# Optimization experiments

Measured on AMD Instinct MI355X. Metric: run time of the kernel, lower is better.

Reference implementation:

```python
import jax, jax.numpy as jnp
import numpy as np

D_EMBED = 64
N_HEADS = 4
D_HEAD = D_EMBED // N_HEADS
D_FF = 96          # int(1.5 * d_embed)
D_MODEL = 128      # repeat_factor = d_model // d_embed = 2
EPS = 1e-5
B = 4
# (idx_start, kernel_size, channels_in, kernel_no) per layer of the source CNN
LAYERS = [(0, 9, 8, 256), (18688, 9, 16, 256), (55808, 9, 16, 512)]
N_PARAMS = 130048
MAX_SEQ = max(ks * cin for _, ks, cin, _ in LAYERS) + 1  # 145


def _kernel_indices(start, ks, cin, kno):
    # Static ragged slice indices: per kernel, its weights plus trailing bias.
    L = ks * cin
    base = start + np.arange(kno)[:, None] * L + np.arange(L)[None, :]
    bias = start + kno * L + np.arange(kno)
    return np.concatenate([base, bias[:, None]], axis=1)  # (kno, L+1)


_IDX = [jnp.asarray(_kernel_indices(*l)) for l in LAYERS]


def setup_inputs():
    key = jax.random.key(0)
    k = jax.random.split(key, 8)
    s = 1.0 / np.sqrt(D_EMBED)
    return {
        "x": jax.random.normal(k[0], (B, N_PARAMS), dtype=jnp.float32),
        "pos_emb": jax.random.normal(k[1], (MAX_SEQ, D_EMBED), dtype=jnp.float32) * s,
        "comp_token": jax.random.normal(k[2], (D_EMBED,), dtype=jnp.float32),
        "in_proj_w": jax.random.normal(k[3], (3 * D_EMBED, D_EMBED), dtype=jnp.float32) * s,
        "in_proj_b": jnp.zeros((3 * D_EMBED,), jnp.float32),
        "out_proj_w": jax.random.normal(k[4], (D_EMBED, D_EMBED), dtype=jnp.float32) * s,
        "out_proj_b": jnp.zeros((D_EMBED,), jnp.float32),
        "lin1_w": jax.random.normal(k[5], (D_FF, D_EMBED), dtype=jnp.float32) * s,
        "lin1_b": jnp.zeros((D_FF,), jnp.float32),
        "lin2_w": jax.random.normal(k[6], (D_EMBED, D_FF), dtype=jnp.float32) / np.sqrt(D_FF),
        "lin2_b": jnp.zeros((D_EMBED,), jnp.float32),
        "ln1_w": jnp.ones((D_EMBED,), jnp.float32),
        "ln1_b": jnp.zeros((D_EMBED,), jnp.float32),
        "ln2_w": jnp.ones((D_EMBED,), jnp.float32),
        "ln2_b": jnp.zeros((D_EMBED,), jnp.float32),
    }


def _layernorm(x, w, b):
    mu = jnp.mean(x, axis=-1, keepdims=True)
    var = jnp.mean(jnp.square(x - mu), axis=-1, keepdims=True)
    return (x - mu) * jax.lax.rsqrt(var + EPS) * w + b


def _encoder(t, in_proj_w, in_proj_b, out_proj_w, out_proj_b,
             lin1_w, lin1_b, lin2_w, lin2_b, ln1_w, ln1_b, ln2_w, ln2_b):
    # Post-norm TransformerEncoderLayer (relu, eval mode -> dropout = identity).
    M, S, _ = t.shape
    qkv = t @ in_proj_w.T + in_proj_b                     # (M, S, 3D)
    q, k, v = jnp.split(qkv, 3, axis=-1)
    heads = lambda u: u.reshape(M, S, N_HEADS, D_HEAD).transpose(0, 2, 1, 3)
    q, k, v = heads(q), heads(k), heads(v)
    attn = jax.nn.softmax(jnp.einsum('mhsd,mhtd->mhst', q, k) / np.sqrt(D_HEAD))
    o = jnp.einsum('mhst,mhtd->mhsd', attn, v).transpose(0, 2, 1, 3).reshape(M, S, D_EMBED)
    o = o @ out_proj_w.T + out_proj_b
    h = _layernorm(t + o, ln1_w, ln1_b)
    ff = jax.nn.relu(h @ lin1_w.T + lin1_b) @ lin2_w.T + lin2_b
    return _layernorm(h + ff, ln2_w, ln2_b)


def reference(x, pos_emb, comp_token, in_proj_w, in_proj_b, out_proj_w, out_proj_b,
              lin1_w, lin1_b, lin2_w, lin2_b, ln1_w, ln1_b, ln2_w, ln2_b):
    enc = (in_proj_w, in_proj_b, out_proj_w, out_proj_b,
           lin1_w, lin1_b, lin2_w, lin2_b, ln1_w, ln1_b, ln2_w, ln2_b)
    outs = []
    for idx in _IDX:  # fixed small loop over layers; kernels within a layer are batched
        K, n = idx.shape
        w = x[:, idx]                                     # (B, K, n) ragged gather
        tok = w[..., None] + pos_emb[:n]                  # scalar -> d_embed broadcast + pos add
        cls = jnp.broadcast_to(comp_token, (B, K, 1, D_EMBED))
        tok = jnp.concatenate([cls, tok], axis=2).reshape(B * K, n + 1, D_EMBED)
        y = _encoder(tok, *enc)[:, 0, :]                  # comp-token readout
        outs.append(y.reshape(B, K, D_EMBED))
    y = jnp.concatenate(outs, axis=1)                     # (B, 1024, d_embed)
    return jnp.tile(y, (1, 1, D_MODEL // D_EMBED))        # (B, 1024, d_model)
```

## Files before the change

### kernel.cpp

```cpp
#include <hip/hip_runtime.h>
#include <math.h>

#define NPAR 130048
#define EPSF 1e-5f

#define VSTR  148
#define WSTR  68
#define L2STR 100

#define OFF_VPOST 0
#define OFF_WO    (64*VSTR)
#define OFF_L1    (OFF_WO + 64*WSTR)
#define OFF_L2    (OFF_L1 + 96*WSTR)
#define OFF_BETA  (OFF_L2 + 64*L2STR)
#define OFF_SM    (OFF_BETA + 4*VSTR)
#define SM_CT   0
#define SM_BO   64
#define SM_B1   128
#define SM_B2   224
#define SM_LN1W 288
#define SM_LN1B 352
#define SM_LN2W 416
#define SM_LN2B 480
#define SM_VCLS 544
#define SM_UV   608
#define SM_ALGA 672
#define SM_SIZE 680
#define SHARED_FLOATS (OFF_SM + SM_SIZE)

#define PW_W    0
#define PW_O    VSTR
#define PW_H1   (VSTR+64)
#define PW_R    (VSTR+128)
#define PW_ATT  (VSTR+224)
#define PW_SIZE (VSTR+224+2*VSTR)
#define LDS_FLOATS (SHARED_FLOATS + 16*PW_SIZE)

#define WSV 0
#define WSB (64*VSTR)
#define WSC (WSB + 4*VSTR)
#define WS_TOTAL (WSC + 136)

#define WAVE_SYNC() asm volatile("s_waitcnt lgkmcnt(0)" ::: "memory")

__device__ __forceinline__ unsigned short f2b(float f) {
    unsigned u = __float_as_uint(f);
    return (unsigned short)((u + 0x7fffu + ((u >> 16) & 1u)) >> 16);
}

__global__ __launch_bounds__(64) void k_pre(const float* __restrict__ pe,
                                            const float* __restrict__ ct,
                                            const float* __restrict__ W,
                                            const float* __restrict__ bq,
                                            float* __restrict__ ws)
{
    const int j = blockIdx.x;
    const int o = threadIdx.x;
    const float4* wq4 = (const float4*)(W + o*64);
    const float4* wk4 = (const float4*)(W + (64 + o)*64);
    const float4* wv4 = (const float4*)(W + (128 + o)*64);
    const float4* ct4 = (const float4*)ct;

    if (j < 145) {
        const float4* p4 = (const float4*)(pe + j*64);
        float sk = bq[64 + o], sv = bq[128 + o], sq = bq[o];
        #pragma unroll
        for (int e = 0; e < 16; ++e) {
            float4 k4 = wk4[e], v4 = wv4[e], q4 = wq4[e], pp = p4[e], cc = ct4[e];
            sk += k4.x*pp.x + k4.y*pp.y + k4.z*pp.z + k4.w*pp.w;
            sv += v4.x*pp.x + v4.y*pp.y + v4.z*pp.z + v4.w*pp.w;
            sq += q4.x*cc.x + q4.y*cc.y + q4.z*cc.z + q4.w*cc.w;
        }
        ws[WSV + o*VSTR + j] = sv;
        float r = sq * sk;
        #pragma unroll
        for (int off = 1; off < 16; off <<= 1) r += __shfl_xor(r, off);
        if ((o & 15) == 0) ws[WSB + (o >> 4)*VSTR + j] = r;
    } else {
        float sq = bq[o], sk = bq[64 + o], sv = bq[128 + o], suk = 0.f, suv = 0.f;
        #pragma unroll
        for (int e = 0; e < 16; ++e) {
            float4 k4 = wk4[e], v4 = wv4[e], q4 = wq4[e], cc = ct4[e];
            sq += q4.x*cc.x + q4.y*cc.y + q4.z*cc.z + q4.w*cc.w;
            sk += k4.x*cc.x + k4.y*cc.y + k4.z*cc.z + k4.w*cc.w;
            sv += v4.x*cc.x + v4.y*cc.y + v4.z*cc.z + v4.w*cc.w;
            suk += k4.x + k4.y + k4.z + k4.w;
            suv += v4.x + v4.y + v4.z + v4.w;
        }
        ws[WSC + o]      = sv;
        ws[WSC + 64 + o] = suv;
        ws[WSV + o*VSTR + 145] = 0.f;
        ws[WSV + o*VSTR + 146] = 0.f;
        ws[WSV + o*VSTR + 147] = 0.f;
        float a = sq * suk, g = sq * sk;
        #pragma unroll
        for (int off = 1; off < 16; off <<= 1) {
            a += __shfl_xor(a, off);
            g += __shfl_xor(g, off);
        }
        if ((o & 15) == 0) { ws[WSC + 128 + (o >> 4)] = a; ws[WSC + 128 + 4 + (o >> 4)] = g; }
    }
}

template<int L>
__device__ __forceinline__ void seq_compute(
    const float* __restrict__ xb, int start, int kno, int k, int lane,
    const float* __restrict__ lds, float* __restrict__ pw,
    float* __restrict__ po)
{
    constexpr int N  = L + 1;
    constexpr int S  = N + 1;
    constexpr int NS = (S + 15) / 16;
    constexpr int N4 = (N + 3) / 4;

    const float* sm = lds + OFF_SM;
    float* w_s = pw + PW_W;
    unsigned short* au = (unsigned short*)(pw + PW_ATT);

    if (lane * 4 < L) {
        float4 v = *(const float4*)(xb + start + (size_t)k * L + lane*4);
        *(float4*)(w_s + lane*4) = v;
    }
    if (lane == 0) w_s[L] = xb[start + (size_t)kno * L + k];
    WAVE_SYNC();

    const int e = lane & 15;
    const int h = lane >> 4;
    const float alpha = sm[SM_ALGA + h];
    const float gam   = sm[SM_ALGA + 4 + h];
    const float* bh   = lds + OFF_BETA + h*VSTR;

    float p[NS];
    float m = -1e30f;
    #pragma unroll
    for (int t = 0; t < NS; ++t) {
        const int s = e + 16*t;
        float v = -1e30f;
        if (s < S) {
            v = (s == 0) ? gam : fmaf(alpha, w_s[s-1], bh[s-1]);
            v *= 0.25f;
        }
        p[t] = v;
        m = fmaxf(m, v);
    }
    #pragma unroll
    for (int off = 1; off < 16; off <<= 1) m = fmaxf(m, __shfl_xor(m, off));

    float sum = 0.f;
    #pragma unroll
    for (int t = 0; t < NS; ++t) {
        const int s = e + 16*t;
        if (s < S) { float ex = __expf(p[t] - m); p[t] = ex; sum += ex; }
    }
    #pragma unroll
    for (int off = 1; off < 16; off <<= 1) sum += __shfl_xor(sum, off);
    const float inv = 1.f / sum;

    float wsl = 0.f;
    #pragma unroll
    for (int t = 0; t < NS; ++t) {
        const int s = e + 16*t;
        if (s > 0 && s < S) {
            float a = p[t] * inv;
            au[h*VSTR + (s-1)] = f2b(a);
            wsl += a * w_s[s-1];
        }
    }
    #pragma unroll
    for (int off = 1; off < 16; off <<= 1) wsl += __shfl_xor(wsl, off);
    const float wsum = wsl;
    const float a0 = __shfl(p[0] * inv, lane & 48);
    { int jj = N + e; if (jj < 4*N4) au[h*VSTR + jj] = 0; }
    WAVE_SYNC();

    const int d = lane;
    {
        const float4* vrow = (const float4*)(lds + OFF_VPOST + d*VSTR);
        const unsigned short* ah = au + h*VSTR;
        float c0 = 0.f, c1 = 0.f, c2 = 0.f, c3 = 0.f;
        #pragma unroll
        for (int t = 0; t < N4; ++t) {
            uint2 aa = *(const uint2*)(ah + 4*t);
            float4 v = vrow[t];
            c0 += __uint_as_float(aa.x << 16)          * v.x;
            c1 += __uint_as_float(aa.x & 0xffff0000u)  * v.y;
            c2 += __uint_as_float(aa.y << 16)          * v.z;
            c3 += __uint_as_float(aa.y & 0xffff0000u)  * v.w;
        }
        pw[PW_O + d] = (c0 + c1) + (c2 + c3) + wsum*sm[SM_UV + d] + a0*sm[SM_VCLS + d];
    }
    WAVE_SYNC();

    float op = sm[SM_BO + d];
    {
        const float4* wr = (const float4*)(lds + OFF_WO + d*WSTR);
        const float4* os = (const float4*)(pw + PW_O);
        float ax=0, ay=0, az=0, aw=0;
        #pragma unroll
        for (int t = 0; t < 16; ++t) {
            float4 w4 = wr[t], o4 = os[t];
            ax += w4.x*o4.x; ay += w4.y*o4.y; az += w4.z*o4.z; aw += w4.w*o4.w;
        }
        op += (ax + ay) + (az + aw);
    }
    float pre = sm[SM_CT + d] + op;
    float mu = pre;
    #pragma unroll
    for (int off = 32; off; off >>= 1) mu += __shfl_xor(mu, off);
    mu *= (1.f/64.f);
    float dv = pre - mu;
    float var = dv*dv;
    #pragma unroll
    for (int off = 32; off; off >>= 1) var += __shfl_xor(var, off);
    var *= (1.f/64.f);
    float h1 = dv * rsqrtf(var + EPSF) * sm[SM_LN1W + d] + sm[SM_LN1B + d];
    pw[PW_H1 + d] = h1;
    WAVE_SYNC();

    {
        const float4* hv = (const float4*)(pw + PW_H1);
        {
            const float4* r1 = (const float4*)(lds + OFF_L1 + lane*WSTR);
            float ax=0, ay=0, az=0, aw=0;
            #pragma unroll
            for (int t = 0; t < 16; ++t) {
                float4 w4 = r1[t], h4 = hv[t];
                ax += w4.x*h4.x; ay += w4.y*h4.y; az += w4.z*h4.z; aw += w4.w*h4.w;
            }
            pw[PW_R + lane] = fmaxf(sm[SM_B1 + lane] + (ax+ay) + (az+aw), 0.f);
        }
        if (lane < 32) {
            const float4* r1 = (const float4*)(lds + OFF_L1 + (64 + lane)*WSTR);
            float ax=0, ay=0, az=0, aw=0;
            #pragma unroll
            for (int t = 0; t < 16; ++t) {
                float4 w4 = r1[t], h4 = hv[t];
                ax += w4.x*h4.x; ay += w4.y*h4.y; az += w4.z*h4.z; aw += w4.w*h4.w;
            }
            pw[PW_R + 64 + lane] = fmaxf(sm[SM_B1 + 64 + lane] + (ax+ay) + (az+aw), 0.f);
        }
    }
    WAVE_SYNC();

    float f2 = sm[SM_B2 + d];
    {
        const float4* r2 = (const float4*)(lds + OFF_L2 + d*L2STR);
        const float4* rv = (const float4*)(pw + PW_R);
        float ax=0, ay=0, az=0, aw=0;
        #pragma unroll
        for (int t = 0; t < 24; ++t) {
            float4 w4 = r2[t], h4 = rv[t];
            ax += w4.x*h4.x; ay += w4.y*h4.y; az += w4.z*h4.z; aw += w4.w*h4.w;
        }
        f2 += (ax + ay) + (az + aw);
    }
    float pre2 = h1 + f2;
    float mu2 = pre2;
    #pragma unroll
    for (int off = 32; off; off >>= 1) mu2 += __shfl_xor(mu2, off);
    mu2 *= (1.f/64.f);
    float dv2 = pre2 - mu2;
    float var2 = dv2*dv2;
    #pragma unroll
    for (int off = 32; off; off >>= 1) var2 += __shfl_xor(var2, off);
    var2 *= (1.f/64.f);
    float y = dv2 * rsqrtf(var2 + EPSF) * sm[SM_LN2W + d] + sm[SM_LN2B + d];

    po[d]      = y;
    po[64 + d] = y;
}

__global__ __launch_bounds__(1024, 4) void k_main(
    const float* __restrict__ x,
    const float* __restrict__ ct,
    const float* __restrict__ Wo,  const float* __restrict__ bo,
    const float* __restrict__ L1w, const float* __restrict__ b1,
    const float* __restrict__ L2w, const float* __restrict__ b2,
    const float* __restrict__ ln1w, const float* __restrict__ ln1b,
    const float* __restrict__ ln2w, const float* __restrict__ ln2b,
    const float* __restrict__ ws,
    float* __restrict__ out)
{
    __shared__ float lds[LDS_FLOATS];
    const int tid = threadIdx.x;

    {
        const float4* s4 = (const float4*)(ws + WSV);
        float4* d4 = (float4*)(lds + OFF_VPOST);
        for (int i = tid; i < 2368; i += 1024) d4[i] = s4[i];
        if (tid < 148) ((float4*)(lds + OFF_BETA))[tid] = ((const float4*)(ws + WSB))[tid];
        for (int idx = tid; idx < 4096; idx += 1024)
            lds[OFF_WO + (idx >> 6)*WSTR + (idx & 63)] = Wo[idx];
        for (int idx = tid; idx < 6144; idx += 1024)
            lds[OFF_L1 + (idx >> 6)*WSTR + (idx & 63)] = L1w[idx];
        for (int idx = tid; idx < 6144; idx += 1024) {
            int r = idx / 96, c = idx - r*96;
            lds[OFF_L2 + r*L2STR + c] = L2w[idx];
        }
        if (tid < 64) {
            lds[OFF_SM + SM_CT   + tid] = ct[tid];
            lds[OFF_SM + SM_BO   + tid] = bo[tid];
            lds[OFF_SM + SM_B2   + tid] = b2[tid];
            lds[OFF_SM + SM_LN1W + tid] = ln1w[tid];
            lds[OFF_SM + SM_LN1B + tid] = ln1b[tid];
            lds[OFF_SM + SM_LN2W + tid] = ln2w[tid];
            lds[OFF_SM + SM_LN2B + tid] = ln2b[tid];
        } else if (tid < 256) {
            int t = tid - 64;
            if (t < 96) lds[OFF_SM + SM_B1 + t] = b1[t];
        } else if (tid < 392) {
            int t = tid - 256;
            lds[OFF_SM + SM_VCLS + t] = ws[WSC + t];
        }
    }
    __syncthreads();

    const int wave = tid >> 6;
    const int lane = tid & 63;
    float* pw = lds + SHARED_FLOATS + wave * PW_SIZE;
    int g = wave * 256 + blockIdx.x;

    if (wave < 4) {
        int b = g >> 8, k = g & 255;
        seq_compute<72>(x + (size_t)b*NPAR, 0, 256, k, lane, lds, pw,
                        out + ((size_t)b*1024 + k)*128);
    } else if (wave < 8) {
        g -= 1024; int b = g >> 8, k = g & 255;
        seq_compute<144>(x + (size_t)b*NPAR, 18688, 256, k, lane, lds, pw,
                         out + ((size_t)b*1024 + 256 + k)*128);
    } else {
        g -= 2048; int b = g >> 9, k = g & 511;
        seq_compute<144>(x + (size_t)b*NPAR, 55808, 512, k, lane, lds, pw,
                         out + ((size_t)b*1024 + 512 + k)*128);
    }
}

extern "C" void kernel_launch(void* const* d_in, const int* in_sizes, int n_in,
                              void* d_out, int out_size, void* d_ws, size_t ws_size,
                              hipStream_t stream) {
    const float* x    = (const float*)d_in[0];
    const float* pe   = (const float*)d_in[1];
    const float* ct   = (const float*)d_in[2];
    const float* Wq   = (const float*)d_in[3];
    const float* bq   = (const float*)d_in[4];
    const float* Wo   = (const float*)d_in[5];
    const float* bo   = (const float*)d_in[6];
    const float* L1w  = (const float*)d_in[7];
    const float* b1   = (const float*)d_in[8];
    const float* L2w  = (const float*)d_in[9];
    const float* b2   = (const float*)d_in[10];
    const float* ln1w = (const float*)d_in[11];
    const float* ln1b = (const float*)d_in[12];
    const float* ln2w = (const float*)d_in[13];
    const float* ln2b = (const float*)d_in[14];
    float* out = (float*)d_out;
    float* ws  = (float*)d_ws;

    k_pre <<<146, 64, 0, stream>>>(pe, ct, Wq, bq, ws);
    k_main<<<256, 1024, 0, stream>>>(x, ct, Wo, bo, L1w, b1, L2w, b2,
                                     ln1w, ln1b, ln2w, ln2b, ws, out);
}
```

Measured before the change: 23.15 us.

## Store weights and activations as fp16 in LDS and use packed dot2

```diff
diff --git a/kernel.cpp b/kernel.cpp
--- a/kernel.cpp
+++ b/kernel.cpp
@@ -4,16 +4,30 @@
 #define NPAR 130048
 #define EPSF 1e-5f
 
-#define VSTR  148
-#define WSTR  68
-#define L2STR 100
+typedef _Float16 hfp;
+typedef _Float16 h2 __attribute__((ext_vector_type(2)));
+
+#if defined(__has_builtin)
+#if __has_builtin(__builtin_amdgcn_fdot2)
+#define FDOT2(a,b,c) __builtin_amdgcn_fdot2((a),(b),(c),false)
+#endif
+#endif
+#ifndef FDOT2
+#define FDOT2(a,b,c) ((float)(a).x*(float)(b).x + (float)(a).y*(float)(b).y + (c))
+#endif
+
+__device__ __forceinline__ h2 f2h2(float f) { union { float f; h2 h; } u; u.f = f; return u.h; }
+
+#define VSTRH  152
+#define WSTRH  72
+#define L2STRH 104
 
 #define OFF_VPOST 0
-#define OFF_WO    (64*VSTR)
-#define OFF_L1    (OFF_WO + 64*WSTR)
-#define OFF_L2    (OFF_L1 + 96*WSTR)
-#define OFF_BETA  (OFF_L2 + 64*L2STR)
-#define OFF_SM    (OFF_BETA + 4*VSTR)
+#define OFF_WO    4864
+#define OFF_L1    7168
+#define OFF_L2    10624
+#define OFF_BETA  13952
+#define OFF_SM    14560
 #define SM_CT   0
 #define SM_BO   64
 #define SM_B1   128
@@ -25,28 +39,21 @@
 #define SM_VCLS 544
 #define SM_UV   608
 #define SM_ALGA 672
-#define SM_SIZE 680
-#define SHARED_FLOATS (OFF_SM + SM_SIZE)
+#define SHARED_FLOATS 15240
 
 #define PW_W    0
-#define PW_O    VSTR
-#define PW_H1   (VSTR+64)
-#define PW_R    (VSTR+128)
-#define PW_ATT  (VSTR+224)
-#define PW_SIZE (VSTR+224+2*VSTR)
+#define PW_O    152
+#define PW_H1   184
+#define PW_R    216
+#define PW_ATT  264
+#define PW_SIZE 568
 #define LDS_FLOATS (SHARED_FLOATS + 16*PW_SIZE)
 
-#define WSV 0
-#define WSB (64*VSTR)
-#define WSC (WSB + 4*VSTR)
-#define WS_TOTAL (WSC + 136)
+#define WSV_F 0
+#define WSB_F 4864
+#define WSC_F 5472
 
 #define WAVE_SYNC() asm volatile("s_waitcnt lgkmcnt(0)" ::: "memory")
-
-__device__ __forceinline__ unsigned short f2b(float f) {
-    unsigned u = __float_as_uint(f);
-    return (unsigned short)((u + 0x7fffu + ((u >> 16) & 1u)) >> 16);
-}
 
 __global__ __launch_bounds__(64) void k_pre(const float* __restrict__ pe,
                                             const float* __restrict__ ct,
@@ -60,6 +67,7 @@
     const float4* wk4 = (const float4*)(W + (64 + o)*64);
     const float4* wv4 = (const float4*)(W + (128 + o)*64);
     const float4* ct4 = (const float4*)ct;
+    hfp* wsh = (hfp*)ws;
 
     if (j < 145) {
         const float4* p4 = (const float4*)(pe + j*64);
@@ -71,11 +79,11 @@
             sv += v4.x*pp.x + v4.y*pp.y + v4.z*pp.z + v4.w*pp.w;
             sq += q4.x*cc.x + q4.y*cc.y + q4.z*cc.z + q4.w*cc.w;
         }
-        ws[WSV + o*VSTR + j] = sv;
+        wsh[o*VSTRH + j] = (hfp)sv;
         float r = sq * sk;
         #pragma unroll
         for (int off = 1; off < 16; off <<= 1) r += __shfl_xor(r, off);
-        if ((o & 15) == 0) ws[WSB + (o >> 4)*VSTR + j] = r;
+        if ((o & 15) == 0) ws[WSB_F + (o >> 4)*152 + j] = r;
     } else {
         float sq = bq[o], sk = bq[64 + o], sv = bq[128 + o], suk = 0.f, suv = 0.f;
         #pragma unroll
@@ -87,48 +95,49 @@
             suk += k4.x + k4.y + k4.z + k4.w;
             suv += v4.x + v4.y + v4.z + v4.w;
         }
-        ws[WSC + o]      = sv;
-        ws[WSC + 64 + o] = suv;
-        ws[WSV + o*VSTR + 145] = 0.f;
-        ws[WSV + o*VSTR + 146] = 0.f;
-        ws[WSV + o*VSTR + 147] = 0.f;
+        ws[WSC_F + o]      = sv;
+        ws[WSC_F + 64 + o] = suv;
+        #pragma unroll
+        for (int jj = 145; jj < VSTRH; ++jj) wsh[o*VSTRH + jj] = (hfp)0.f;
         float a = sq * suk, g = sq * sk;
         #pragma unroll
         for (int off = 1; off < 16; off <<= 1) {
             a += __shfl_xor(a, off);
             g += __shfl_xor(g, off);
         }
-        if ((o & 15) == 0) { ws[WSC + 128 + (o >> 4)] = a; ws[WSC + 128 + 4 + (o >> 4)] = g; }
+        if ((o & 15) == 0) { ws[WSC_F + 128 + (o >> 4)] = a; ws[WSC_F + 128 + 4 + (o >> 4)] = g; }
     }
 }
 
 template<int L>
 __device__ __forceinline__ void seq_compute(
-    const float* __restrict__ xb, int start, int kno, int k, int lane,
-    const float* __restrict__ lds, float* __restrict__ pw,
+    float4 wv, float wb, int lane,
+    float* __restrict__ lds, float* __restrict__ pw,
     float* __restrict__ po)
 {
     constexpr int N  = L + 1;
     constexpr int S  = N + 1;
     constexpr int NS = (S + 15) / 16;
-    constexpr int N4 = (N + 3) / 4;
+    constexpr int N8 = ((N + 7) / 8) * 8;
+    constexpr int NT = N8 / 8;
 
     const float* sm = lds + OFF_SM;
+    const hfp* ldsh = (const hfp*)lds;
     float* w_s = pw + PW_W;
-    unsigned short* au = (unsigned short*)(pw + PW_ATT);
-
-    if (lane * 4 < L) {
-        float4 v = *(const float4*)(xb + start + (size_t)k * L + lane*4);
-        *(float4*)(w_s + lane*4) = v;
-    }
-    if (lane == 0) w_s[L] = xb[start + (size_t)kno * L + k];
+    hfp* oh  = (hfp*)(pw + PW_O);
+    hfp* h1h = (hfp*)(pw + PW_H1);
+    hfp* rh  = (hfp*)(pw + PW_R);
+    hfp* att = (hfp*)(pw + PW_ATT);
+
+    if (lane * 4 < L) *(float4*)(w_s + lane*4) = wv;
+    if (lane == 0) w_s[L] = wb;
     WAVE_SYNC();
 
     const int e = lane & 15;
     const int h = lane >> 4;
     const float alpha = sm[SM_ALGA + h];
     const float gam   = sm[SM_ALGA + 4 + h];
-    const float* bh   = lds + OFF_BETA + h*VSTR;
+    const float* bh   = lds + OFF_BETA + h*152;
 
     float p[NS];
     float m = -1e30f;
@@ -162,7 +171,7 @@
         const int s = e + 16*t;
         if (s > 0 && s < S) {
             float a = p[t] * inv;
-            au[h*VSTR + (s-1)] = f2b(a);
+            att[h*VSTRH + (s-1)] = (hfp)a;
             wsl += a * w_s[s-1];
         }
     }
@@ -170,38 +179,41 @@
     for (int off = 1; off < 16; off <<= 1) wsl += __shfl_xor(wsl, off);
     const float wsum = wsl;
     const float a0 = __shfl(p[0] * inv, lane & 48);
-    { int jj = N + e; if (jj < 4*N4) au[h*VSTR + jj] = 0; }
+    { int jj = N + e; if (jj < N8) att[h*VSTRH + jj] = (hfp)0.f; }
     WAVE_SYNC();
 
     const int d = lane;
     {
-        const float4* vrow = (const float4*)(lds + OFF_VPOST + d*VSTR);
-        const unsigned short* ah = au + h*VSTR;
+        const float4* vrow = (const float4*)(ldsh + d*VSTRH);
+        const float4* arow = (const float4*)(att + h*VSTRH);
         float c0 = 0.f, c1 = 0.f, c2 = 0.f, c3 = 0.f;
         #pragma unroll
-        for (int t = 0; t < N4; ++t) {
-            uint2 aa = *(const uint2*)(ah + 4*t);
-            float4 v = vrow[t];
-            c0 += __uint_as_float(aa.x << 16)          * v.x;
-            c1 += __uint_as_float(aa.x & 0xffff0000u)  * v.y;
-            c2 += __uint_as_float(aa.y << 16)          * v.z;
-            c3 += __uint_as_float(aa.y & 0xffff0000u)  * v.w;
-        }
-        pw[PW_O + d] = (c0 + c1) + (c2 + c3) + wsum*sm[SM_UV + d] + a0*sm[SM_VCLS + d];
+        for (int t = 0; t < NT; ++t) {
+            float4 av = arow[t], vvv = vrow[t];
+            c0 = FDOT2(f2h2(av.x), f2h2(vvv.x), c0);
+            c1 = FDOT2(f2h2(av.y), f2h2(vvv.y), c1);
+            c2 = FDOT2(f2h2(av.z), f2h2(vvv.z), c2);
+            c3 = FDOT2(f2h2(av.w), f2h2(vvv.w), c3);
+        }
+        float ov = (c0 + c1) + (c2 + c3) + wsum*sm[SM_UV + d] + a0*sm[SM_VCLS + d];
+        oh[d] = (hfp)ov;
     }
     WAVE_SYNC();
 
     float op = sm[SM_BO + d];
     {
-        const float4* wr = (const float4*)(lds + OFF_WO + d*WSTR);
-        const float4* os = (const float4*)(pw + PW_O);
-        float ax=0, ay=0, az=0, aw=0;
-        #pragma unroll
-        for (int t = 0; t < 16; ++t) {
-            float4 w4 = wr[t], o4 = os[t];
-            ax += w4.x*o4.x; ay += w4.y*o4.y; az += w4.z*o4.z; aw += w4.w*o4.w;
-        }
-        op += (ax + ay) + (az + aw);
+        const float4* wr = (const float4*)(ldsh + OFF_WO*2 + d*WSTRH);
+        const float4* ov = (const float4*)oh;
+        float c0 = 0.f, c1 = 0.f, c2 = 0.f, c3 = 0.f;
+        #pragma unroll
+        for (int t = 0; t < 8; ++t) {
+            float4 w4 = wr[t], o4 = ov[t];
+            c0 = FDOT2(f2h2(w4.x), f2h2(o4.x), c0);
+            c1 = FDOT2(f2h2(w4.y), f2h2(o4.y), c1);
+            c2 = FDOT2(f2h2(w4.z), f2h2(o4.z), c2);
+            c3 = FDOT2(f2h2(w4.w), f2h2(o4.w), c3);
+        }
+        op += (c0 + c1) + (c2 + c3);
     }
     float pre = sm[SM_CT + d] + op;
     float mu = pre;
@@ -214,45 +226,54 @@
     for (int off = 32; off; off >>= 1) var += __shfl_xor(var, off);
     var *= (1.f/64.f);
     float h1 = dv * rsqrtf(var + EPSF) * sm[SM_LN1W + d] + sm[SM_LN1B + d];
-    pw[PW_H1 + d] = h1;
-    WAVE_SYNC();
-
-    {
-        const float4* hv = (const float4*)(pw + PW_H1);
+    h1h[d] = (hfp)h1;
+    WAVE_SYNC();
+
+    {
+        const float4* hv = (const float4*)h1h;
         {
-            const float4* r1 = (const float4*)(lds + OFF_L1 + lane*WSTR);
-            float ax=0, ay=0, az=0, aw=0;
+            const float4* r1 = (const float4*)(ldsh + OFF_L1*2 + lane*WSTRH);
+            float c0 = 0.f, c1 = 0.f, c2 = 0.f, c3 = 0.f;
             #pragma unroll
-            for (int t = 0; t < 16; ++t) {
+            for (int t = 0; t < 8; ++t) {
                 float4 w4 = r1[t], h4 = hv[t];
-                ax += w4.x*h4.x; ay += w4.y*h4.y; az += w4.z*h4.z; aw += w4.w*h4.w;
+                c0 = FDOT2(f2h2(w4.x), f2h2(h4.x), c0);
+                c1 = FDOT2(f2h2(w4.y), f2h2(h4.y), c1);
+                c2 = FDOT2(f2h2(w4.z), f2h2(h4.z), c2);
+                c3 = FDOT2(f2h2(w4.w), f2h2(h4.w), c3);
             }
-            pw[PW_R + lane] = fmaxf(sm[SM_B1 + lane] + (ax+ay) + (az+aw), 0.f);
+            rh[lane] = (hfp)fmaxf(sm[SM_B1 + lane] + (c0+c1) + (c2+c3), 0.f);
         }
         if (lane < 32) {
-            const float4* r1 = (const float4*)(lds + OFF_L1 + (64 + lane)*WSTR);
-            float ax=0, ay=0, az=0, aw=0;
+            const float4* r1 = (const float4*)(ldsh + OFF_L1*2 + (64 + lane)*WSTRH);
+            float c0 = 0.f, c1 = 0.f, c2 = 0.f, c3 = 0.f;
             #pragma unroll
-            for (int t = 0; t < 16; ++t) {
+            for (int t = 0; t < 8; ++t) {
                 float4 w4 = r1[t], h4 = hv[t];
-                ax += w4.x*h4.x; ay += w4.y*h4.y; az += w4.z*h4.z; aw += w4.w*h4.w;
+                c0 = FDOT2(f2h2(w4.x), f2h2(h4.x), c0);
+                c1 = FDOT2(f2h2(w4.y), f2h2(h4.y), c1);
+                c2 = FDOT2(f2h2(w4.z), f2h2(h4.z), c2);
+                c3 = FDOT2(f2h2(w4.w), f2h2(h4.w), c3);
             }
-            pw[PW_R + 64 + lane] = fmaxf(sm[SM_B1 + 64 + lane] + (ax+ay) + (az+aw), 0.f);
+            rh[64 + lane] = (hfp)fmaxf(sm[SM_B1 + 64 + lane] + (c0+c1) + (c2+c3), 0.f);
         }
     }
     WAVE_SYNC();
 
     float f2 = sm[SM_B2 + d];
     {
-        const float4* r2 = (const float4*)(lds + OFF_L2 + d*L2STR);
-        const float4* rv = (const float4*)(pw + PW_R);
-        float ax=0, ay=0, az=0, aw=0;
-        #pragma unroll
-        for (int t = 0; t < 24; ++t) {
+        const float4* r2 = (const float4*)(ldsh + OFF_L2*2 + d*L2STRH);
+        const float4* rv = (const float4*)rh;
+        float c0 = 0.f, c1 = 0.f, c2 = 0.f, c3 = 0.f;
+        #pragma unroll
+        for (int t = 0; t < 12; ++t) {
             float4 w4 = r2[t], h4 = rv[t];
-            ax += w4.x*h4.x; ay += w4.y*h4.y; az += w4.z*h4.z; aw += w4.w*h4.w;
-        }
-        f2 += (ax + ay) + (az + aw);
+            c0 = FDOT2(f2h2(w4.x), f2h2(h4.x), c0);
+            c1 = FDOT2(f2h2(w4.y), f2h2(h4.y), c1);
+            c2 = FDOT2(f2h2(w4.z), f2h2(h4.z), c2);
+            c3 = FDOT2(f2h2(w4.w), f2h2(h4.w), c3);
+        }
+        f2 += (c0 + c1) + (c2 + c3);
     }
     float pre2 = h1 + f2;
     float mu2 = pre2;
@@ -282,20 +303,33 @@
     float* __restrict__ out)
 {
     __shared__ float lds[LDS_FLOATS];
-    const int tid = threadIdx.x;
-
-    {
-        const float4* s4 = (const float4*)(ws + WSV);
+    const int tid  = threadIdx.x;
+    const int wave = tid >> 6;
+    const int lane = tid & 63;
+
+    int g = wave * 256 + blockIdx.x;
+    int start, L, kno, k, outidx, b;
+    if (wave < 4)       { b = g >> 8; k = g & 255;            start = 0;     L = 72;  kno = 256; outidx = b*1024 + k; }
+    else if (wave < 8)  { g -= 1024; b = g >> 8; k = g & 255; start = 18688; L = 144; kno = 256; outidx = b*1024 + 256 + k; }
+    else                { g -= 2048; b = g >> 9; k = g & 511; start = 55808; L = 144; kno = 512; outidx = b*1024 + 512 + k; }
+    const float* xb = x + (size_t)b * NPAR;
+    float4 wv = make_float4(0.f, 0.f, 0.f, 0.f);
+    if (lane * 4 < L) wv = *(const float4*)(xb + start + (size_t)k * L + lane*4);
+    float wb = (lane == 0) ? xb[start + (size_t)kno * L + k] : 0.f;
+
+    {
+        hfp* ldsh = (hfp*)lds;
+        const float4* s4 = (const float4*)(ws + WSV_F);
         float4* d4 = (float4*)(lds + OFF_VPOST);
-        for (int i = tid; i < 2368; i += 1024) d4[i] = s4[i];
-        if (tid < 148) ((float4*)(lds + OFF_BETA))[tid] = ((const float4*)(ws + WSB))[tid];
+        for (int i = tid; i < 1216; i += 1024) d4[i] = s4[i];
+        if (tid < 152) ((float4*)(lds + OFF_BETA))[tid] = ((const float4*)(ws + WSB_F))[tid];
         for (int idx = tid; idx < 4096; idx += 1024)
-            lds[OFF_WO + (idx >> 6)*WSTR + (idx & 63)] = Wo[idx];
+            ldsh[OFF_WO*2 + (idx >> 6)*WSTRH + (idx & 63)] = (hfp)Wo[idx];
         for (int idx = tid; idx < 6144; idx += 1024)
-            lds[OFF_L1 + (idx >> 6)*WSTR + (idx & 63)] = L1w[idx];
+            ldsh[OFF_L1*2 + (idx >> 6)*WSTRH + (idx & 63)] = (hfp)L1w[idx];
         for (int idx = tid; idx < 6144; idx += 1024) {
             int r = idx / 96, c = idx - r*96;
-            lds[OFF_L2 + r*L2STR + c] = L2w[idx];
+            ldsh[OFF_L2*2 + r*L2STRH + c] = (hfp)L2w[idx];
         }
         if (tid < 64) {
             lds[OFF_SM + SM_CT   + tid] = ct[tid];
@@ -310,29 +344,16 @@
             if (t < 96) lds[OFF_SM + SM_B1 + t] = b1[t];
         } else if (tid < 392) {
             int t = tid - 256;
-            lds[OFF_SM + SM_VCLS + t] = ws[WSC + t];
+            lds[OFF_SM + SM_VCLS + t] = ws[WSC_F + t];
         }
     }
     __syncthreads();
 
-    const int wave = tid >> 6;
-    const int lane = tid & 63;
     float* pw = lds + SHARED_FLOATS + wave * PW_SIZE;
-    int g = wave * 256 + blockIdx.x;
-
-    if (wave < 4) {
-        int b = g >> 8, k = g & 255;
-        seq_compute<72>(x + (size_t)b*NPAR, 0, 256, k, lane, lds, pw,
-                        out + ((size_t)b*1024 + k)*128);
-    } else if (wave < 8) {
-        g -= 1024; int b = g >> 8, k = g & 255;
-        seq_compute<144>(x + (size_t)b*NPAR, 18688, 256, k, lane, lds, pw,
-                         out + ((size_t)b*1024 + 256 + k)*128);
-    } else {
-        g -= 2048; int b = g >> 9, k = g & 511;
-        seq_compute<144>(x + (size_t)b*NPAR, 55808, 512, k, lane, lds, pw,
-                         out + ((size_t)b*1024 + 512 + k)*128);
-    }
+    float* po = out + (size_t)outidx * 128;
+
+    if (wave < 4) seq_compute<72>(wv, wb, lane, lds, pw, po);
+    else          seq_compute<144>(wv, wb, lane, lds, pw, po);
 }
 
 extern "C" void kernel_launch(void* const* d_in, const int* in_sizes, int n_in,
```

New measurement: 20.11 us. 1.15x faster.
